# Kernel tuning notes

Measured on AMD Instinct MI355X. Metric: run time of the kernel, lower is better.

## Reference

```python
import jax, jax.numpy as jnp
import numpy as np

B, S, D, U = 4, 2048, 1024, 1024

def setup_inputs() -> dict:
    key = jax.random.key(0)
    k0, k1, k2, k3 = jax.random.split(key, 4)
    scale = 1.0 / np.sqrt(D)  # keep logits sane; Glorot-like magnitude
    return {
        "inputs": jax.random.normal(k0, (B, S, D), dtype=jnp.float32),
        "W_q": jax.random.normal(k1, (D, U), dtype=jnp.float32) * scale,
        "W_k": jax.random.normal(k2, (D, U), dtype=jnp.float32) * scale,
        "W_v": jax.random.normal(k3, (D, U), dtype=jnp.float32) * scale,
    }

def reference(inputs, W_q, W_k, W_v):
    # QKV projections: [B,S,D] @ [D,U] -> [B,S,U]
    q = jnp.einsum("bsd,du->bsu", inputs, W_q)
    k = jnp.einsum("bsd,du->bsu", inputs, W_k)
    v = jnp.einsum("bsd,du->bsu", inputs, W_v)
    # Unscaled attention, as in the source (no 1/sqrt(d) factor)
    scores = jnp.einsum("bqu,bku->bqk", q, k)          # [B,S,S]
    weights = jax.nn.softmax(scores, axis=-1)
    return jnp.einsum("bqk,bku->bqu", weights, v)       # [B,S,U]
```

## Files before the change

kernel.cpp:

```cpp
#include <hip/hip_runtime.h>
#include <cstdint>
#include <cstddef>


typedef unsigned short ushort_t;
typedef _Float16 half_t;
typedef __attribute__((ext_vector_type(8))) short short8;
typedef __attribute__((ext_vector_type(4))) float floatx4;

__device__ inline unsigned short h2u(half_t h) {
  union { half_t h; unsigned short u; } v; v.h = h; return v.u;
}

__device__ __forceinline__ void gload16(const half_t* g, half_t* l) {
  __builtin_amdgcn_global_load_lds(
      (const __attribute__((address_space(1))) unsigned int*)g,
      (__attribute__((address_space(3))) unsigned int*)l, 16, 0, 0);
}

#define BAR() asm volatile("s_barrier" ::: "memory")
#define LGKM0() asm volatile("s_waitcnt lgkmcnt(0)" ::: "memory")
#define VM6() asm volatile("s_waitcnt vmcnt(6)" ::: "memory")
#define VM0() asm volatile("s_waitcnt vmcnt(0)" ::: "memory")

#define MX 8192
#define KCAT 2048

#define XCAT_OFF 0UL
#define WT_OFF   50331648UL
#define S_OFF    0UL
#define QCAT_OFF 69206016UL
#define KCAT_OFF 119537664UL
#define VT_OFF   169869312UL
#define WS_NEED  186646528UL

#define XCD_REMAP(BX, BY, BZ)                                              \
  const int fbid_ = blockIdx.x + 8 * (blockIdx.y + gridDim.y * blockIdx.z); \
  const int xj_ = fbid_ & 7, xi_ = fbid_ >> 3;                              \
  const int BX = ((xj_ & 1) << 2) | (xi_ & 3);                              \
  const int nrow_ = (xj_ >> 1) * ((gridDim.y * gridDim.z) >> 2) + (xi_ >> 2);\
  const int BY = nrow_ % gridDim.y;                                         \
  const int BZ = nrow_ / gridDim.y;

__global__ __launch_bounds__(256) void k_split_x(const float* __restrict__ X,
                                                 half_t* __restrict__ xcat) {
  long long i = (long long)blockIdx.x * 256 + threadIdx.x;
  float x = X[i];
  half_t h = (half_t)x;
  half_t lo = (half_t)(x - (float)h);
  long long row = i >> 10;
  int col = (int)(i & 1023);
  half_t* r = xcat + row * KCAT;
  r[col] = h;
  r[col + 1024] = lo;
}

__global__ __launch_bounds__(256) void k_split_wt(const float* __restrict__ Wq,
                                                  const float* __restrict__ Wk,
                                                  const float* __restrict__ Wv,
                                                  half_t* __restrict__ wt) {
  __shared__ float tile[64][65];
  const float* W = (blockIdx.z == 0) ? Wq : ((blockIdx.z == 1) ? Wk : Wv);
  half_t* out = wt + (size_t)blockIdx.z * 1024 * KCAT;
  int d0 = blockIdx.y * 64, u0 = blockIdx.x * 64;
  int t = threadIdx.x;
  int tr = t >> 6, tc = t & 63;
  for (int r = 0; r < 64; r += 4)
    tile[r + tr][tc] = W[(size_t)(d0 + r + tr) * 1024 + (u0 + tc)];
  __syncthreads();
  for (int r = 0; r < 64; r += 4) {
    int urow = r + tr, dcol = tc;
    float x = tile[dcol][urow];
    half_t h = (half_t)x;
    half_t* o = out + (size_t)(u0 + urow) * KCAT + d0;
    o[dcol] = h;
    o[dcol + 1024] = h;
  }
}

enum { EP_F32 = 0, EP_QK = 1, EP_VT = 2 };

template <int MODE>
__global__ __launch_bounds__(256, 4) void k_gemm(
    const half_t* __restrict__ A, long long aBatch, int lda,
    const half_t* __restrict__ Bt, long long bBatch, int ldb,
    void* __restrict__ Cout, long long cBatch, int ldc, int K,
    half_t* __restrict__ CoutK) {
  __shared__ __align__(16) half_t As[128 * 64];
  __shared__ __align__(16) half_t Bs[128 * 64];
  const int t = threadIdx.x;
  XCD_REMAP(bx, by, z);
  A += (long long)z * aBatch;
  Bt += (long long)z * bBatch;
  const int m0 = by * 128, n0 = bx * 128;

  const int w = t >> 6, l = t & 63;
  const int lr = l & 15, quad = l >> 4;
  const int wm = (w >> 1) * 64, wn = (w & 1) * 64;

  const floatx4 fz = {0.f, 0.f, 0.f, 0.f};
  floatx4 acc[4][4];
#pragma unroll
  for (int i = 0; i < 4; i++)
#pragma unroll
    for (int j = 0; j < 4; j++) acc[i][j] = fz;

  const half_t* Ap[4];
  const half_t* Bp[4];
  half_t* ldsA[4];
  half_t* ldsB[4];
#pragma unroll
  for (int s = 0; s < 4; s++) {
    int c = s * 256 + t;
    int row = c >> 3, gq = (c & 7) ^ ((c >> 3) & 7);
    Ap[s] = A + (long long)(m0 + row) * lda + gq * 8;
    Bp[s] = Bt + (long long)(n0 + row) * ldb + gq * 8;
    ldsA[s] = &As[(s * 256 + w * 64) * 8];
    ldsB[s] = &Bs[(s * 256 + w * 64) * 8];
  }

  const int p0 = quad ^ (lr & 7);
  const int p1 = (quad + 4) ^ (lr & 7);
  const int arow = (wm + lr) * 64, brow = (wn + lr) * 64;

  for (int kb = 0; kb < K; kb += 64) {
    __syncthreads();
#pragma unroll
    for (int s = 0; s < 4; s++) {
      gload16(Ap[s] + kb, ldsA[s]);
      gload16(Bp[s] + kb, ldsB[s]);
    }
    __syncthreads();
#pragma unroll
    for (int s = 0; s < 2; s++) {
      const int pp = s ? p1 : p0;
      short8 af[4], bfg[4];
#pragma unroll
      for (int j = 0; j < 4; j++) bfg[j] = *(const short8*)&Bs[brow + j * 1024 + pp * 8];
#pragma unroll
      for (int i = 0; i < 4; i++) af[i] = *(const short8*)&As[arow + i * 1024 + pp * 8];
#pragma unroll
      for (int i = 0; i < 4; i++)
#pragma unroll
        for (int j = 0; j < 4; j++)
          acc[i][j] = __builtin_amdgcn_mfma_f32_16x16x32_f16(af[i], bfg[j], acc[i][j], 0, 0, 0);
    }
  }

#pragma unroll
  for (int i = 0; i < 4; i++) {
#pragma unroll
    for (int j = 0; j < 4; j++) {
#pragma unroll
      for (int r = 0; r < 4; r++) {
        int grow = m0 + wm + i * 16 + quad * 4 + r;
        int gcol = n0 + wn + j * 16 + lr;
        float v = acc[i][j][r];
        if (MODE == EP_F32) {
          float* C = (float*)Cout + (long long)z * cBatch;
          C[(long long)grow * ldc + gcol] = v;
        } else {
          half_t* C = (half_t*)Cout;
          int b = grow >> 11, s = grow & 2047;
          C[((long long)b * 1024 + gcol) * 2048 + s] = (half_t)v;
        }
      }
    }
  }
}

template <int MODE>
__global__ __launch_bounds__(512, 2) void k_gemm256(
    const half_t* __restrict__ A, long long aBatch, int lda,
    const half_t* __restrict__ Bt, long long bBatch, int ldb,
    void* __restrict__ Cout, long long cBatch, int ldc, int K,
    half_t* __restrict__ CoutK) {
  __shared__ __align__(16) half_t As[32768];
  __shared__ __align__(16) half_t Bs[32768];
  const int tid = threadIdx.x;
  XCD_REMAP(bx, by, z);
  A += (long long)z * aBatch;
  Bt += (long long)z * bBatch;
  const int m0 = by * 256, n0 = bx * 256;
  const int w = tid >> 6, l = tid & 63;
  const int lr = l & 15, quad = l >> 4;
  const int wm = w >> 2, wn = w & 3;

  const floatx4 fz = {0.f, 0.f, 0.f, 0.f};
  floatx4 acc[8][4];
#pragma unroll
  for (int i = 0; i < 8; i++)
#pragma unroll
    for (int j = 0; j < 4; j++) acc[i][j] = fz;

  const int r0 = tid >> 2;
  const int gq0 = (tid & 3) ^ ((tid >> 3) & 3);
  const half_t* aS0 = A + (long long)(m0 + r0) * lda + gq0 * 8;
  const half_t* aS1 = aS0 + (long long)128 * lda;
  const half_t* bS0 = Bt + (long long)(n0 + r0) * ldb + gq0 * 8;
  const half_t* bS1 = bS0 + (long long)128 * ldb;
  const int wso = w << 9;

  const int swz = (quad ^ ((lr >> 1) & 3)) << 3;
  const int aBase = wm * 4096 + lr * 32 + swz;
  const int bBase = wn * 2048 + lr * 32 + swz;
  const int NT = K >> 6;

#define SA(BUF, KH, KOFF) do { half_t* d_ = &As[(BUF) * 16384 + (KH) * 8192 + wso]; \
    gload16(aS0 + (KOFF), d_); gload16(aS1 + (KOFF), d_ + 4096); } while (0)
#define SB(BUF, KH, KOFF) do { half_t* d_ = &Bs[(BUF) * 16384 + (KH) * 8192 + wso]; \
    gload16(bS0 + (KOFF), d_); gload16(bS1 + (KOFF), d_ + 4096); } while (0)
#define LDA4(S, OFF) { const half_t* ap_ = &As[(OFF)]; \
    S##0 = *(const short8*)(ap_); S##1 = *(const short8*)(ap_ + 512); \
    S##2 = *(const short8*)(ap_ + 1024); S##3 = *(const short8*)(ap_ + 1536); }
#define LDB4(S, OFF) { const half_t* bp_ = &Bs[(OFF)]; \
    S##0 = *(const short8*)(bp_); S##1 = *(const short8*)(bp_ + 512); \
    S##2 = *(const short8*)(bp_ + 1024); S##3 = *(const short8*)(bp_ + 1536); }
#define MFMA16(I0, AS, BS) do { \
    acc[(I0) + 0][0] = __builtin_amdgcn_mfma_f32_16x16x32_f16(AS##0, BS##0, acc[(I0) + 0][0], 0, 0, 0); \
    acc[(I0) + 0][1] = __builtin_amdgcn_mfma_f32_16x16x32_f16(AS##0, BS##1, acc[(I0) + 0][1], 0, 0, 0); \
    acc[(I0) + 0][2] = __builtin_amdgcn_mfma_f32_16x16x32_f16(AS##0, BS##2, acc[(I0) + 0][2], 0, 0, 0); \
    acc[(I0) + 0][3] = __builtin_amdgcn_mfma_f32_16x16x32_f16(AS##0, BS##3, acc[(I0) + 0][3], 0, 0, 0); \
    acc[(I0) + 1][0] = __builtin_amdgcn_mfma_f32_16x16x32_f16(AS##1, BS##0, acc[(I0) + 1][0], 0, 0, 0); \
    acc[(I0) + 1][1] = __builtin_amdgcn_mfma_f32_16x16x32_f16(AS##1, BS##1, acc[(I0) + 1][1], 0, 0, 0); \
    acc[(I0) + 1][2] = __builtin_amdgcn_mfma_f32_16x16x32_f16(AS##1, BS##2, acc[(I0) + 1][2], 0, 0, 0); \
    acc[(I0) + 1][3] = __builtin_amdgcn_mfma_f32_16x16x32_f16(AS##1, BS##3, acc[(I0) + 1][3], 0, 0, 0); \
    acc[(I0) + 2][0] = __builtin_amdgcn_mfma_f32_16x16x32_f16(AS##2, BS##0, acc[(I0) + 2][0], 0, 0, 0); \
    acc[(I0) + 2][1] = __builtin_amdgcn_mfma_f32_16x16x32_f16(AS##2, BS##1, acc[(I0) + 2][1], 0, 0, 0); \
    acc[(I0) + 2][2] = __builtin_amdgcn_mfma_f32_16x16x32_f16(AS##2, BS##2, acc[(I0) + 2][2], 0, 0, 0); \
    acc[(I0) + 2][3] = __builtin_amdgcn_mfma_f32_16x16x32_f16(AS##2, BS##3, acc[(I0) + 2][3], 0, 0, 0); \
    acc[(I0) + 3][0] = __builtin_amdgcn_mfma_f32_16x16x32_f16(AS##3, BS##0, acc[(I0) + 3][0], 0, 0, 0); \
    acc[(I0) + 3][1] = __builtin_amdgcn_mfma_f32_16x16x32_f16(AS##3, BS##1, acc[(I0) + 3][1], 0, 0, 0); \
    acc[(I0) + 3][2] = __builtin_amdgcn_mfma_f32_16x16x32_f16(AS##3, BS##2, acc[(I0) + 3][2], 0, 0, 0); \
    acc[(I0) + 3][3] = __builtin_amdgcn_mfma_f32_16x16x32_f16(AS##3, BS##3, acc[(I0) + 3][3], 0, 0, 0); \
  } while (0)

  short8 aA0, aA1, aA2, aA3;
  short8 aB0, aB1, aB2, aB3;
  short8 bA0, bA1, bA2, bA3;
  short8 bB0, bB1, bB2, bB3;

  SB(0, 0, 0); SA(0, 0, 0); SB(0, 1, 32); SA(0, 1, 32);
  SB(1, 0, 64); SA(1, 0, 64); SB(1, 1, 96);
  VM6();
  BAR();
  LDA4(aA, aBase);
  LDB4(bA, bBase);

  for (int t = 0; t < NT; ++t) {
    const int buf = t & 1, nbuf = buf ^ 1;
    const int ab = buf * 16384, nab = nbuf * 16384;
    const int kb = t * 64;

    LDA4(aB, ab + aBase + 2048);
    if (t + 1 < NT) SA(nbuf, 1, kb + 96);
    BAR();
    __builtin_amdgcn_s_setprio(1); MFMA16(0, aA, bA); __builtin_amdgcn_s_setprio(0);
    BAR();

    LDA4(aA, ab + 8192 + aBase);
    LDB4(bB, ab + 8192 + bBase);
    if (t + 2 < NT) SB(buf, 0, kb + 128);
    BAR();
    __builtin_amdgcn_s_setprio(1); MFMA16(4, aB, bA); __builtin_amdgcn_s_setprio(0);
    BAR();

    LDA4(aB, ab + 8192 + aBase + 2048);
    if (t + 2 < NT) SA(buf, 0, kb + 128);
    BAR();
    __builtin_amdgcn_s_setprio(1); MFMA16(0, aA, bB); __builtin_amdgcn_s_setprio(0);
    BAR();

    if (t + 2 < NT) SB(buf, 1, kb + 160);
    if (t < NT - 2) { VM6(); } else if (t == NT - 2) { VM0(); }
    BAR();
    __builtin_amdgcn_s_setprio(1); MFMA16(4, aB, bB); __builtin_amdgcn_s_setprio(0);
    if (t + 1 < NT) {
      LDA4(aA, nab + aBase);
      LDB4(bA, nab + bBase);
    }
    BAR();
  }

#pragma unroll
  for (int i = 0; i < 8; i++) {
#pragma unroll
    for (int j = 0; j < 4; j++) {
#pragma unroll
      for (int r = 0; r < 4; r++) {
        int grow = m0 + wm * 128 + i * 16 + quad * 4 + r;
        int gcol = n0 + wn * 64 + j * 16 + lr;
        float v = acc[i][j][r];
        if (MODE == EP_F32) {
          float* C = (float*)Cout + (long long)z * cBatch;
          C[(long long)grow * ldc + gcol] = v;
        } else {
          int sel = gcol >> 10;
          int ucol = gcol & 1023;
          half_t h = (half_t)v;
          unsigned hu = h2u(h);
          unsigned val;
          half_t* base;
          if (sel == 0) {
            val = hu | ((unsigned)h2u((half_t)(v - (float)h)) << 16);
            base = (half_t*)Cout;
          } else {
            val = hu | (hu << 16);
            base = CoutK;
          }
          *(unsigned*)(base + (long long)grow * KCAT + 2 * ucol) = val;
        }
      }
    }
  }
#undef SA
#undef SB
#undef LDA4
#undef LDB4
#undef MFMA16
}

__global__ __launch_bounds__(256) void k_softmax(float* __restrict__ Sbuf) {
  long long row = blockIdx.x;
  float* p = Sbuf + row * 2048;
  int t = threadIdx.x;
  float4 v0 = ((const float4*)p)[t];
  float4 v1 = ((const float4*)p)[t + 256];
  float m = fmaxf(fmaxf(fmaxf(v0.x, v0.y), fmaxf(v0.z, v0.w)),
                  fmaxf(fmaxf(v1.x, v1.y), fmaxf(v1.z, v1.w)));
  for (int off = 32; off; off >>= 1) m = fmaxf(m, __shfl_xor(m, off));
  __shared__ float red[8];
  int wv = t >> 6, ln = t & 63;
  if (ln == 0) red[wv] = m;
  __syncthreads();
  m = fmaxf(fmaxf(red[0], red[1]), fmaxf(red[2], red[3]));
  float e0 = __expf(v0.x - m), e1 = __expf(v0.y - m), e2 = __expf(v0.z - m), e3 = __expf(v0.w - m);
  float e4 = __expf(v1.x - m), e5 = __expf(v1.y - m), e6 = __expf(v1.z - m), e7 = __expf(v1.w - m);
  float s = ((e0 + e1) + (e2 + e3)) + ((e4 + e5) + (e6 + e7));
  for (int off = 32; off; off >>= 1) s += __shfl_xor(s, off);
  if (ln == 0) red[4 + wv] = s;
  __syncthreads();
  s = (red[4] + red[5]) + (red[6] + red[7]);
  float inv = 1.0f / s;
  uint2 w0, w1;
  w0.x = (unsigned)h2u((half_t)(e0 * inv)) | ((unsigned)h2u((half_t)(e1 * inv)) << 16);
  w0.y = (unsigned)h2u((half_t)(e2 * inv)) | ((unsigned)h2u((half_t)(e3 * inv)) << 16);
  w1.x = (unsigned)h2u((half_t)(e4 * inv)) | ((unsigned)h2u((half_t)(e5 * inv)) << 16);
  w1.y = (unsigned)h2u((half_t)(e6 * inv)) | ((unsigned)h2u((half_t)(e7 * inv)) << 16);
  ((uint2*)p)[t] = w0;
  ((uint2*)p)[t + 256] = w1;
}

extern "C" void kernel_launch(void* const* d_in, const int* in_sizes, int n_in,
                              void* d_out, int out_size, void* d_ws, size_t ws_size,
                              hipStream_t stream) {
  (void)in_sizes; (void)n_in; (void)out_size;
  if (ws_size < WS_NEED) return;

  const float* X = (const float*)d_in[0];
  const float* Wq = (const float*)d_in[1];
  const float* Wk = (const float*)d_in[2];
  const float* Wv = (const float*)d_in[3];
  char* ws = (char*)d_ws;
  half_t* xcat = (half_t*)(ws + XCAT_OFF);
  half_t* wt = (half_t*)(ws + WT_OFF);
  float* Sbuf = (float*)(ws + S_OFF);
  half_t* qcat = (half_t*)(ws + QCAT_OFF);
  half_t* kcat = (half_t*)(ws + KCAT_OFF);
  half_t* vt = (half_t*)(ws + VT_OFF);
  float* out = (float*)d_out;

  k_split_x<<<dim3(MX * 1024 / 256), dim3(256), 0, stream>>>(X, xcat);
  k_split_wt<<<dim3(16, 16, 3), dim3(256), 0, stream>>>(Wq, Wk, Wv, wt);

  k_gemm256<EP_QK><<<dim3(8, 32, 1), dim3(512), 0, stream>>>(
      xcat, 0LL, KCAT, wt, 0LL, KCAT, qcat, 0LL, 0, KCAT, kcat);

  k_gemm<EP_VT><<<dim3(8, 64, 1), dim3(256), 0, stream>>>(
      xcat, 0LL, KCAT, wt + 2 * 1024 * KCAT, 0LL, KCAT, vt, 0LL, 0, 1024, nullptr);

  k_gemm256<EP_F32><<<dim3(8, 8, 4), dim3(512), 0, stream>>>(
      qcat, (long long)2048 * KCAT, KCAT, kcat, (long long)2048 * KCAT, KCAT,
      Sbuf, (long long)2048 * 2048, 2048, KCAT, nullptr);

  k_softmax<<<dim3(8192), dim3(256), 0, stream>>>(Sbuf);

  k_gemm<EP_F32><<<dim3(8, 16, 4), dim3(256), 0, stream>>>(
      (const half_t*)Sbuf, (long long)2048 * 4096, 4096,
      vt, (long long)1024 * 2048, 2048,
      out, (long long)2048 * 1024, 1024, 2048, nullptr);
}
```

Baseline: 317.5 us.

## Restructure GEMM main loop into two half-K phases with batched LDS loads

The K-loop in the MFMA GEMM is reorganized from four quarter-phases with register double-buffering into two half-phases. Each phase loads all A and B fragments for its 32-wide K slice from LDS, then issues 32 MFMAs. Global-to-LDS prefetches are regrouped in A/B pairs, and the vmcnt waits change from 6 to 8 or 4. This aims to cut barriers per iteration and lengthen uninterrupted MFMA runs. In exchange, it gives up overlap between LDS reads and MFMA execution and uses more fragment registers at once.

```diff
diff --git a/kernel.cpp b/kernel.cpp
--- a/kernel.cpp
+++ b/kernel.cpp
@@ -20,7 +20,8 @@
 
 #define BAR() asm volatile("s_barrier" ::: "memory")
 #define LGKM0() asm volatile("s_waitcnt lgkmcnt(0)" ::: "memory")
-#define VM6() asm volatile("s_waitcnt vmcnt(6)" ::: "memory")
+#define VM8() asm volatile("s_waitcnt vmcnt(8)" ::: "memory")
+#define VM4() asm volatile("s_waitcnt vmcnt(4)" ::: "memory")
 #define VM0() asm volatile("s_waitcnt vmcnt(0)" ::: "memory")
 
 #define MX 8192
@@ -235,51 +236,55 @@
     acc[(I0) + 3][3] = __builtin_amdgcn_mfma_f32_16x16x32_f16(AS##3, BS##3, acc[(I0) + 3][3], 0, 0, 0); \
   } while (0)
 
-  short8 aA0, aA1, aA2, aA3;
-  short8 aB0, aB1, aB2, aB3;
-  short8 bA0, bA1, bA2, bA3;
-  short8 bB0, bB1, bB2, bB3;
-
   SB(0, 0, 0); SA(0, 0, 0); SB(0, 1, 32); SA(0, 1, 32);
-  SB(1, 0, 64); SA(1, 0, 64); SB(1, 1, 96);
-  VM6();
+  SA(1, 0, 64); SB(1, 0, 64);
+  VM8();
   BAR();
-  LDA4(aA, aBase);
-  LDB4(bA, bBase);
 
   for (int t = 0; t < NT; ++t) {
     const int buf = t & 1, nbuf = buf ^ 1;
-    const int ab = buf * 16384, nab = nbuf * 16384;
+    const int ab = buf * 16384;
     const int kb = t * 64;
 
-    LDA4(aB, ab + aBase + 2048);
-    if (t + 1 < NT) SA(nbuf, 1, kb + 96);
-    BAR();
-    __builtin_amdgcn_s_setprio(1); MFMA16(0, aA, bA); __builtin_amdgcn_s_setprio(0);
-    BAR();
-
-    LDA4(aA, ab + 8192 + aBase);
-    LDB4(bB, ab + 8192 + bBase);
-    if (t + 2 < NT) SB(buf, 0, kb + 128);
-    BAR();
-    __builtin_amdgcn_s_setprio(1); MFMA16(4, aB, bA); __builtin_amdgcn_s_setprio(0);
-    BAR();
-
-    LDA4(aB, ab + 8192 + aBase + 2048);
-    if (t + 2 < NT) SA(buf, 0, kb + 128);
-    BAR();
-    __builtin_amdgcn_s_setprio(1); MFMA16(0, aA, bB); __builtin_amdgcn_s_setprio(0);
-    BAR();
-
-    if (t + 2 < NT) SB(buf, 1, kb + 160);
-    if (t < NT - 2) { VM6(); } else if (t == NT - 2) { VM0(); }
-    BAR();
-    __builtin_amdgcn_s_setprio(1); MFMA16(4, aB, bB); __builtin_amdgcn_s_setprio(0);
-    if (t + 1 < NT) {
-      LDA4(aA, nab + aBase);
-      LDB4(bA, nab + bBase);
-    }
-    BAR();
+    {
+      short8 aA0, aA1, aA2, aA3, aB0, aB1, aB2, aB3, bA0, bA1, bA2, bA3;
+      LDA4(aA, ab + aBase);
+      LDA4(aB, ab + aBase + 2048);
+      LDB4(bA, ab + bBase);
+      if (t + 1 < NT) {
+        SA(nbuf, 1, kb + 96);
+        SB(nbuf, 1, kb + 96);
+        VM8();
+      } else {
+        VM0();
+      }
+      BAR(); LGKM0();
+      __builtin_amdgcn_s_setprio(1);
+      MFMA16(0, aA, bA);
+      MFMA16(4, aB, bA);
+      __builtin_amdgcn_s_setprio(0);
+      BAR();
+    }
+
+    {
+      short8 aA0, aA1, aA2, aA3, aB0, aB1, aB2, aB3, bA0, bA1, bA2, bA3;
+      LDA4(aA, ab + 8192 + aBase);
+      LDA4(aB, ab + 8192 + aBase + 2048);
+      LDB4(bA, ab + 8192 + bBase);
+      if (t + 2 < NT) {
+        SA(buf, 0, kb + 128);
+        SB(buf, 0, kb + 128);
+        VM8();
+      } else if (t + 1 < NT) {
+        VM4();
+      }
+      BAR(); LGKM0();
+      __builtin_amdgcn_s_setprio(1);
+      MFMA16(0, aA, bA);
+      MFMA16(4, aB, bA);
+      __builtin_amdgcn_s_setprio(0);
+      BAR();
+    }
   }
 
 #pragma unroll
```

After: 315.0 us. No clear change (-0.8%).
